# Performance work log

Hardware: AMD Instinct MI355X
Metric: run time of the kernel (lower is better)

Reference implementation:

```python
import jax, jax.numpy as jnp
import numpy as np

N_NODES = 50000
N_EDGES = 600000
D = 128
H = 256  # backbone hidden
EPS = 1e-5
NEG_SLOPE = 0.01


def setup_inputs() -> dict:
    key = jax.random.key(0)
    ks = jax.random.split(key, 16)
    s = 0.05
    inp = {
        "x": jax.random.normal(ks[0], (N_NODES, D), dtype=jnp.float32),
        "edges": jax.random.randint(ks[1], (2, N_EDGES), 0, N_NODES, dtype=jnp.int64),
        # merge layer: Linear(2D -> D), stored as (in, out)
        "merge_W": jax.random.normal(ks[2], (2 * D, D), dtype=jnp.float32) * s,
        "merge_b": jnp.zeros((D,), dtype=jnp.float32),
        # GRUCell params, torch layout: (3D, D) rows ordered [r, z, n]
        "gru_W_ih": jax.random.normal(ks[3], (3 * D, D), dtype=jnp.float32) * s,
        "gru_W_hh": jax.random.normal(ks[4], (3 * D, D), dtype=jnp.float32) * s,
        "gru_b_ih": jnp.zeros((3 * D,), dtype=jnp.float32),
        "gru_b_hh": jnp.zeros((3 * D,), dtype=jnp.float32),
        # backbone: Linear(D->256) + LeakyReLU + BN(256) + Linear(256->D) + LeakyReLU + BN(D)
        "W1": jax.random.normal(ks[5], (D, H), dtype=jnp.float32) * s,
        "b1": jnp.zeros((H,), dtype=jnp.float32),
        "gamma1": jnp.ones((H,), dtype=jnp.float32),
        "beta1": jnp.zeros((H,), dtype=jnp.float32),
        "W2": jax.random.normal(ks[6], (H, D), dtype=jnp.float32) * s,
        "b2": jnp.zeros((D,), dtype=jnp.float32),
        "gamma2": jnp.ones((D,), dtype=jnp.float32),
        "beta2": jnp.zeros((D,), dtype=jnp.float32),
    }
    return inp


def _batch_norm(y, gamma, beta):
    m = jnp.mean(y, axis=0)
    v = jnp.mean((y - m) ** 2, axis=0)  # biased var, training mode
    return gamma * (y - m) * jax.lax.rsqrt(v + EPS) + beta


def _leaky_relu(y):
    return jnp.where(y >= 0, y, NEG_SLOPE * y)


def reference(x, edges, merge_W, merge_b, gru_W_ih, gru_W_hh, gru_b_ih, gru_b_hh,
              W1, b1, gamma1, beta1, W2, b2, gamma2, beta2):
    n = x.shape[0]
    src, dst = edges[0], edges[1]
    x_neighbor = x[src]  # (E, D) gather

    # aggregation: 'sum' and 'max' scatter reductions over center nodes
    agg_sum = jax.ops.segment_sum(x_neighbor, dst, num_segments=n)
    agg_max = jax.ops.segment_max(x_neighbor, dst, num_segments=n)
    agg_max = jnp.where(jnp.isfinite(agg_max), agg_max, 0.0)  # nodes with no in-edges -> 0

    # merge multiple aggregations: cat + Linear(2D -> D)
    agg = jnp.concatenate([agg_sum, agg_max], axis=-1) @ merge_W + merge_b

    # update: GRUCell(input=agg, hidden=x)
    gi = agg @ gru_W_ih.T + gru_b_ih
    gh = x @ gru_W_hh.T + gru_b_hh
    i_r, i_z, i_n = jnp.split(gi, 3, axis=-1)
    h_r, h_z, h_n = jnp.split(gh, 3, axis=-1)
    r = jax.nn.sigmoid(i_r + h_r)
    z = jax.nn.sigmoid(i_z + h_z)
    cand = jnp.tanh(i_n + r * h_n)
    h = (1.0 - z) * cand + z * x

    # backbone MLP with training-mode BatchNorm
    y = _batch_norm(_leaky_relu(h @ W1 + b1), gamma1, beta1)
    y = _batch_norm(_leaky_relu(y @ W2 + b2), gamma2, beta2)
    return y
```

## Files before the change

### kernel.cpp

```cpp
#include <hip/hip_runtime.h>
#include <hip/hip_bf16.h>
#include <math.h>

#define NN 50000
#define NE 600000
#define DD 128
#define HH 256
#define BN_EPS 1e-5f

typedef unsigned short u16;
typedef short bf16x8 __attribute__((ext_vector_type(8)));
typedef float f32x4 __attribute__((ext_vector_type(4)));

__device__ __forceinline__ u16 f2bf(float f) {
    unsigned int u = __float_as_uint(f);
    unsigned int r = (u + 0x7fffu + ((u >> 16) & 1u)) >> 16;
    return (u16)r;
}
__device__ __forceinline__ float bf2f(u16 b) {
    return __uint_as_float(((unsigned int)b) << 16);
}
#define MFMA(a, b, c) __builtin_amdgcn_mfma_f32_16x16x32_bf16((a), (b), (c), 0, 0, 0)

__global__ __launch_bounds__(256) void k_init(int* __restrict__ deg,
                                              float* __restrict__ stats) {
    int tid = blockIdx.x * 256 + threadIdx.x;
    if (tid < NN) deg[tid] = 0;
    if (tid < 768) stats[tid] = 0.f;
}

__global__ __launch_bounds__(256) void k_count(const int* __restrict__ edges,
                                               int* __restrict__ deg) {
    int e = blockIdx.x * 256 + threadIdx.x;
    if (e >= NE) return;
    atomicAdd(&deg[edges[NE + e]], 1);
}

__global__ __launch_bounds__(256) void k_scanA(const int* __restrict__ deg,
                                               int* __restrict__ loc,
                                               int* __restrict__ bsum) {
    __shared__ int s[256];
    int b = blockIdx.x, t = threadIdx.x;
    int i0 = b * 512 + t * 2;
    int d0 = (i0 < NN) ? deg[i0] : 0;
    int d1 = (i0 + 1 < NN) ? deg[i0 + 1] : 0;
    s[t] = d0 + d1;
    __syncthreads();
    for (int off = 1; off < 256; off <<= 1) {
        int v = (t >= off) ? s[t - off] : 0;
        __syncthreads();
        s[t] += v;
        __syncthreads();
    }
    int excl = (t > 0) ? s[t - 1] : 0;
    if (i0 < NN) loc[i0] = excl;
    if (i0 + 1 < NN) loc[i0 + 1] = excl + d0;
    if (t == 255) bsum[b] = s[255];
}

__global__ __launch_bounds__(128) void k_scanB(const int* __restrict__ bsum,
                                               int* __restrict__ boff) {
    __shared__ int s[128];
    int t = threadIdx.x;
    const int NBLK = (NN + 511) / 512;
    s[t] = (t < NBLK) ? bsum[t] : 0;
    __syncthreads();
    for (int off = 1; off < 128; off <<= 1) {
        int v = (t >= off) ? s[t - off] : 0;
        __syncthreads();
        s[t] += v;
        __syncthreads();
    }
    if (t < NBLK) boff[t] = (t > 0) ? s[t - 1] : 0;
}

__global__ __launch_bounds__(256) void k_scanC(const int* __restrict__ loc,
                                               const int* __restrict__ boff,
                                               int* __restrict__ rowptr,
                                               int* __restrict__ cursor) {
    int i = blockIdx.x * 256 + threadIdx.x;
    if (i < NN) {
        int v = loc[i] + boff[i >> 9];
        rowptr[i] = v;
        cursor[i] = v;
    }
    if (i == 0) rowptr[NN] = NE;
}

__global__ __launch_bounds__(256) void k_fill(const int* __restrict__ edges,
                                              int* __restrict__ cursor,
                                              int* __restrict__ eidx) {
    int e = blockIdx.x * 256 + threadIdx.x;
    if (e >= NE) return;
    int src = edges[e];
    int dst = edges[NE + e];
    int slot = atomicAdd(&cursor[dst], 1);
    eidx[slot] = src;
}

__global__ __launch_bounds__(256) void k_xcast(const float4* __restrict__ x4,
                                               uint4* __restrict__ xb4) {
    int tid = blockIdx.x * 256 + threadIdx.x;
    if (tid >= NN * DD / 8) return;
    float4 a = x4[tid * 2];
    float4 b = x4[tid * 2 + 1];
    uint4 o;
    o.x = (unsigned)f2bf(a.x) | ((unsigned)f2bf(a.y) << 16);
    o.y = (unsigned)f2bf(a.z) | ((unsigned)f2bf(a.w) << 16);
    o.z = (unsigned)f2bf(b.x) | ((unsigned)f2bf(b.y) << 16);
    o.w = (unsigned)f2bf(b.z) | ((unsigned)f2bf(b.w) << 16);
    xb4[tid] = o;
}

__global__ __launch_bounds__(256) void k_aggregate(const unsigned* __restrict__ xb,
        const int* __restrict__ rowptr, const int* __restrict__ eidx,
        unsigned* __restrict__ asum, unsigned* __restrict__ amax) {
    int gid = blockIdx.x * 256 + threadIdx.x;
    int node = gid >> 6;
    int lane = threadIdx.x & 63;
    if (node >= NN) return;
    int beg = rowptr[node], end = rowptr[node + 1];
    float sx = 0.f, sy = 0.f;
    const float NINF = -__builtin_inff();
    float mx = NINF, my = NINF;
    int j = beg;
    for (; j + 4 <= end; j += 4) {
        int i0 = eidx[j], i1 = eidx[j + 1], i2 = eidx[j + 2], i3 = eidx[j + 3];
        unsigned v0 = xb[(size_t)i0 * 64 + lane];
        unsigned v1 = xb[(size_t)i1 * 64 + lane];
        unsigned v2 = xb[(size_t)i2 * 64 + lane];
        unsigned v3 = xb[(size_t)i3 * 64 + lane];
        float a0 = bf2f((u16)(v0 & 0xffff)), b0 = bf2f((u16)(v0 >> 16));
        float a1 = bf2f((u16)(v1 & 0xffff)), b1 = bf2f((u16)(v1 >> 16));
        float a2 = bf2f((u16)(v2 & 0xffff)), b2 = bf2f((u16)(v2 >> 16));
        float a3 = bf2f((u16)(v3 & 0xffff)), b3 = bf2f((u16)(v3 >> 16));
        sx += a0 + a1 + a2 + a3;
        sy += b0 + b1 + b2 + b3;
        mx = fmaxf(fmaxf(fmaxf(mx, a0), fmaxf(a1, a2)), a3);
        my = fmaxf(fmaxf(fmaxf(my, b0), fmaxf(b1, b2)), b3);
    }
    for (; j < end; ++j) {
        int src = eidx[j];
        unsigned v = xb[(size_t)src * 64 + lane];
        float vx = bf2f((u16)(v & 0xffff));
        float vy = bf2f((u16)(v >> 16));
        sx += vx; sy += vy;
        mx = fmaxf(mx, vx); my = fmaxf(my, vy);
    }
    if (beg == end) { mx = 0.f; my = 0.f; }
    asum[(size_t)node * 64 + lane] = (unsigned)f2bf(sx) | ((unsigned)f2bf(sy) << 16);
    amax[(size_t)node * 64 + lane] = (unsigned)f2bf(mx) | ((unsigned)f2bf(my) << 16);
}

__device__ __forceinline__ size_t packB(int k, int n, int KT) {
    int nt = n >> 4;
    int kt = k >> 5;
    int lane = (n & 15) | (((k >> 3) & 3) << 4);
    int e = k & 7;
    return ((size_t)(nt * KT + kt) * 64 + lane) * 8 + e;
}

__global__ __launch_bounds__(256) void k_prep_w(const float* __restrict__ merge_W,
        const float* __restrict__ W_ih, const float* __restrict__ W_hh,
        const float* __restrict__ merge_b,
        const float* __restrict__ b_ih, const float* __restrict__ b_hh,
        const float* __restrict__ W1,
        u16* __restrict__ Wp, float* __restrict__ bg, u16* __restrict__ W1p) {
    int bid = blockIdx.x, t = threadIdx.x;
    if (bid < 768) {
        int tid = bid * 256 + t;
        int k = tid >> 9;
        int jout = tid & 511;
        float v = 0.f;
        if (jout < 256) {
            int j = jout;
            if (k < 256) {
                float acc = 0.f;
                for (int q = 0; q < DD; ++q) acc += merge_W[k * DD + q] * W_ih[j * DD + q];
                v = acc;
            } else v = W_hh[j * DD + (k - 256)];
        } else if (jout < 384) {
            int j = jout;
            if (k < 256) {
                float acc = 0.f;
                for (int q = 0; q < DD; ++q) acc += merge_W[k * DD + q] * W_ih[j * DD + q];
                v = acc;
            }
        } else {
            int j = jout - 128;
            if (k >= 256) v = W_hh[j * DD + (k - 256)];
        }
        Wp[packB(k, jout, 12)] = f2bf(v);
    } else if (bid < 770) {
        int jout = (bid - 768) * 256 + t;
        float v;
        if (jout < 384) {
            int j = jout;
            float acc = b_ih[j];
            for (int q = 0; q < DD; ++q) acc += merge_b[q] * W_ih[j * DD + q];
            v = (jout < 256) ? acc + b_hh[j] : acc;
        } else {
            v = b_hh[jout - 128];
        }
        bg[jout] = v;
    } else {
        int tid = (bid - 770) * 256 + t;
        int k = tid >> 8;
        int j = tid & 255;
        W1p[packB(k, j, 4)] = f2bf(W1[tid]);
    }
}

__global__ __launch_bounds__(256) void k_gru_mlp1(const u16* __restrict__ asum,
        const u16* __restrict__ amax, const u16* __restrict__ xb,
        const u16* __restrict__ Wp, const float* __restrict__ bg,
        const u16* __restrict__ W1p, const float* __restrict__ b1,
        u16* __restrict__ s1, float* __restrict__ sum1, float* __restrict__ sumsq1) {
    __shared__ u16 U[32 * 392];
    __shared__ u16 HS[32 * 136];
    int t = threadIdx.x;
    int r0 = blockIdx.x * 32;
    int w = t >> 6, l = t & 63;

    #pragma unroll
    for (int src = 0; src < 3; ++src) {
        const u16* p = (src == 0) ? asum : (src == 1) ? amax : xb;
        #pragma unroll
        for (int it = 0; it < 2; ++it) {
            int i = t + it * 256;
            int row = i >> 4, c = i & 15;
            uint4 v = make_uint4(0, 0, 0, 0);
            if (r0 + row < NN) v = *(const uint4*)(p + (size_t)(r0 + row) * DD + c * 8);
            *(uint4*)(&U[row * 392 + src * DD + c * 8]) = v;
        }
    }
    __syncthreads();

    {
        f32x4 acc[2][4][2];
        #pragma unroll
        for (int mt = 0; mt < 2; ++mt)
            #pragma unroll
            for (int g = 0; g < 4; ++g)
                #pragma unroll
                for (int q = 0; q < 2; ++q) acc[mt][g][q] = (f32x4){0.f, 0.f, 0.f, 0.f};

        for (int kt = 0; kt < 12; ++kt) {
            bf16x8 a0 = *(const bf16x8*)(&U[((l & 15)) * 392 + kt * 32 + (l >> 4) * 8]);
            bf16x8 a1 = *(const bf16x8*)(&U[(16 + (l & 15)) * 392 + kt * 32 + (l >> 4) * 8]);
            #pragma unroll
            for (int g = 0; g < 4; ++g) {
                #pragma unroll
                for (int q = 0; q < 2; ++q) {
                    int nt = g * 8 + 2 * w + q;
                    bf16x8 b = *(const bf16x8*)(Wp + ((size_t)(nt * 12 + kt) * 64 + l) * 8);
                    acc[0][g][q] = MFMA(a0, b, acc[0][g][q]);
                    acc[1][g][q] = MFMA(a1, b, acc[1][g][q]);
                }
            }
        }

        #pragma unroll
        for (int mt = 0; mt < 2; ++mt) {
            #pragma unroll
            for (int q = 0; q < 2; ++q) {
                int dl = (2 * w + q) * 16 + (l & 15);
                float br = bg[dl], bz = bg[128 + dl], bi = bg[256 + dl], bh = bg[384 + dl];
                #pragma unroll
                for (int j = 0; j < 4; ++j) {
                    int row = mt * 16 + (l >> 4) * 4 + j;
                    float rp = acc[mt][0][q][j] + br;
                    float zp = acc[mt][1][q][j] + bz;
                    float ip = acc[mt][2][q][j] + bi;
                    float hp = acc[mt][3][q][j] + bh;
                    float r = 1.f / (1.f + __expf(-rp));
                    float z = 1.f / (1.f + __expf(-zp));
                    float n = tanhf(ip + r * hp);
                    float xv = bf2f(U[row * 392 + 2 * DD + dl]);
                    float h = (1.f - z) * n + z * xv;
                    HS[row * 136 + dl] = f2bf(h);
                }
            }
        }
    }
    __syncthreads();

    {
        f32x4 acc[2][4];
        #pragma unroll
        for (int mt = 0; mt < 2; ++mt)
            #pragma unroll
            for (int nl = 0; nl < 4; ++nl) acc[mt][nl] = (f32x4){0.f, 0.f, 0.f, 0.f};

        for (int kt = 0; kt < 4; ++kt) {
            bf16x8 a0 = *(const bf16x8*)(&HS[((l & 15)) * 136 + kt * 32 + (l >> 4) * 8]);
            bf16x8 a1 = *(const bf16x8*)(&HS[(16 + (l & 15)) * 136 + kt * 32 + (l >> 4) * 8]);
            #pragma unroll
            for (int nl = 0; nl < 4; ++nl) {
                int nt = w * 4 + nl;
                bf16x8 b = *(const bf16x8*)(W1p + ((size_t)(nt * 4 + kt) * 64 + l) * 8);
                acc[0][nl] = MFMA(a0, b, acc[0][nl]);
                acc[1][nl] = MFMA(a1, b, acc[1][nl]);
            }
        }

        #pragma unroll
        for (int nl = 0; nl < 4; ++nl) {
            int dcol = (w * 4 + nl) * 16 + (l & 15);
            float bj = b1[dcol];
            float cs = 0.f, cq = 0.f;
            #pragma unroll
            for (int mt = 0; mt < 2; ++mt) {
                #pragma unroll
                for (int j = 0; j < 4; ++j) {
                    int row = mt * 16 + (l >> 4) * 4 + j;
                    float v = acc[mt][nl][j] + bj;
                    v = (v >= 0.f) ? v : 0.01f * v;
                    if (r0 + row < NN) {
                        s1[(size_t)(r0 + row) * HH + dcol] = f2bf(v);
                        cs += v; cq += v * v;
                    }
                }
            }
            cs += __shfl_xor(cs, 16); cs += __shfl_xor(cs, 32);
            cq += __shfl_xor(cq, 16); cq += __shfl_xor(cq, 32);
            if (l < 16) {
                atomicAdd(&sum1[dcol], cs);
                atomicAdd(&sumsq1[dcol], cq);
            }
        }
    }
}

__global__ __launch_bounds__(256) void k_prep2(const float* __restrict__ sum1,
        const float* __restrict__ sumsq1,
        const float* __restrict__ gamma1, const float* __restrict__ beta1,
        const float* __restrict__ W2, const float* __restrict__ b2,
        u16* __restrict__ W2p, float* __restrict__ b2p) {
    __shared__ float a1s[HH], c1s[HH];
    int t = threadIdx.x;
    {
        float m = sum1[t] * (1.f / NN);
        float var = sumsq1[t] * (1.f / NN) - m * m;
        float a = gamma1[t] * rsqrtf(var + BN_EPS);
        a1s[t] = a;
        c1s[t] = beta1[t] - a * m;
    }
    __syncthreads();
    if (blockIdx.x < 128) {
        int idx = blockIdx.x * 256 + t;
        int k = idx >> 7, j = idx & 127;
        W2p[packB(k, j, 8)] = f2bf(a1s[k] * W2[k * DD + j]);
    } else if (t < DD) {
        float acc = b2[t];
        for (int k = 0; k < HH; ++k) acc = fmaf(c1s[k], W2[k * DD + t], acc);
        b2p[t] = acc;
    }
}

__global__ __launch_bounds__(256) void k_mlp2(const u16* __restrict__ s1,
        const u16* __restrict__ W2p, const float* __restrict__ b2p,
        float* __restrict__ s2, float* __restrict__ sum2, float* __restrict__ sumsq2) {
    __shared__ u16 A[32 * 264];
    int t = threadIdx.x;
    int r0 = blockIdx.x * 32;
    int w = t >> 6, l = t & 63;

    #pragma unroll
    for (int it = 0; it < 4; ++it) {
        int i = t + it * 256;
        int row = i >> 5, c = i & 31;
        uint4 v = make_uint4(0, 0, 0, 0);
        if (r0 + row < NN) v = *(const uint4*)(s1 + (size_t)(r0 + row) * HH + c * 8);
        *(uint4*)(&A[row * 264 + c * 8]) = v;
    }
    __syncthreads();

    f32x4 acc[2][2];
    #pragma unroll
    for (int mt = 0; mt < 2; ++mt)
        #pragma unroll
        for (int q = 0; q < 2; ++q) acc[mt][q] = (f32x4){0.f, 0.f, 0.f, 0.f};

    for (int kt = 0; kt < 8; ++kt) {
        bf16x8 a0 = *(const bf16x8*)(&A[((l & 15)) * 264 + kt * 32 + (l >> 4) * 8]);
        bf16x8 a1 = *(const bf16x8*)(&A[(16 + (l & 15)) * 264 + kt * 32 + (l >> 4) * 8]);
        #pragma unroll
        for (int q = 0; q < 2; ++q) {
            int nt = w * 2 + q;
            bf16x8 b = *(const bf16x8*)(W2p + ((size_t)(nt * 8 + kt) * 64 + l) * 8);
            acc[0][q] = MFMA(a0, b, acc[0][q]);
            acc[1][q] = MFMA(a1, b, acc[1][q]);
        }
    }

    #pragma unroll
    for (int q = 0; q < 2; ++q) {
        int dcol = (w * 2 + q) * 16 + (l & 15);
        float bj = b2p[dcol];
        float cs = 0.f, cq = 0.f;
        #pragma unroll
        for (int mt = 0; mt < 2; ++mt) {
            #pragma unroll
            for (int j = 0; j < 4; ++j) {
                int row = mt * 16 + (l >> 4) * 4 + j;
                float v = acc[mt][q][j] + bj;
                v = (v >= 0.f) ? v : 0.01f * v;
                if (r0 + row < NN) {
                    s2[(size_t)(r0 + row) * DD + dcol] = v;
                    cs += v; cq += v * v;
                }
            }
        }
        cs += __shfl_xor(cs, 16); cs += __shfl_xor(cs, 32);
        cq += __shfl_xor(cq, 16); cq += __shfl_xor(cq, 32);
        if (l < 16) {
            atomicAdd(&sum2[dcol], cs);
            atomicAdd(&sumsq2[dcol], cq);
        }
    }
}

__global__ __launch_bounds__(256) void k_bn_out(const float* __restrict__ s2,
        const float* __restrict__ sum2, const float* __restrict__ sumsq2,
        const float* __restrict__ gamma2, const float* __restrict__ beta2,
        float* __restrict__ out) {
    __shared__ float a2s[DD], c2s[DD];
    int t = threadIdx.x;
    if (t < DD) {
        float m = sum2[t] * (1.f / NN);
        float var = sumsq2[t] * (1.f / NN) - m * m;
        float a = gamma2[t] * rsqrtf(var + BN_EPS);
        a2s[t] = a;
        c2s[t] = beta2[t] - a * m;
    }
    __syncthreads();
    int tid = blockIdx.x * 256 + t;
    if (tid >= NN * DD / 4) return;
    int c4 = (tid & 31) * 4;
    float4 v = ((const float4*)s2)[tid];
    float4 o;
    o.x = a2s[c4 + 0] * v.x + c2s[c4 + 0];
    o.y = a2s[c4 + 1] * v.y + c2s[c4 + 1];
    o.z = a2s[c4 + 2] * v.z + c2s[c4 + 2];
    o.w = a2s[c4 + 3] * v.w + c2s[c4 + 3];
    ((float4*)out)[tid] = o;
}

extern "C" void kernel_launch(void* const* d_in, const int* in_sizes, int n_in,
                              void* d_out, int out_size, void* d_ws, size_t ws_size,
                              hipStream_t stream) {
    const float* x       = (const float*)d_in[0];
    const int*   edges   = (const int*)d_in[1];
    const float* merge_W = (const float*)d_in[2];
    const float* merge_b = (const float*)d_in[3];
    const float* W_ih    = (const float*)d_in[4];
    const float* W_hh    = (const float*)d_in[5];
    const float* b_ih    = (const float*)d_in[6];
    const float* b_hh    = (const float*)d_in[7];
    const float* W1      = (const float*)d_in[8];
    const float* b1      = (const float*)d_in[9];
    const float* gamma1  = (const float*)d_in[10];
    const float* beta1   = (const float*)d_in[11];
    const float* W2      = (const float*)d_in[12];
    const float* b2      = (const float*)d_in[13];
    const float* gamma2  = (const float*)d_in[14];
    const float* beta2   = (const float*)d_in[15];
    float* out = (float*)d_out;

    char* wsb = (char*)d_ws;
    u16*   xb     = (u16*)(wsb + 0);
    u16*   asumb  = (u16*)(wsb + 12800000);
    u16*   amaxb  = (u16*)(wsb + 25600000);
    float* s2     = (float*)(wsb + 12800000);
    u16*   s1b    = (u16*)(wsb + 38400000);
    u16*   Wpg    = (u16*)(wsb + 64000000);
    u16*   W1p    = (u16*)(wsb + 64393216);
    u16*   W2p    = (u16*)(wsb + 64458752);
    float* bg     = (float*)(wsb + 64524288);
    float* b2p    = (float*)(wsb + 64526336);
    float* stats  = (float*)(wsb + 64526848);
    float* sum1   = stats;
    float* sumsq1 = stats + 256;
    float* sum2   = stats + 512;
    float* sumsq2 = stats + 640;
    int*   deg    = (int*)(wsb + 64529920);
    int*   rowptr = (int*)(wsb + 64729920);
    int*   cursor = (int*)(wsb + 64929924);
    int*   eidx   = (int*)(wsb + 65129924);
    int*   bsum   = (int*)(wsb + 67529924);
    int*   boff   = (int*)(wsb + 67530316);

    const int NB = (NN + 31) / 32;
    const int NBLK = (NN + 511) / 512;

    k_init<<<(NN + 255) / 256, 256, 0, stream>>>(deg, stats);
    k_count<<<(NE + 255) / 256, 256, 0, stream>>>(edges, deg);
    k_scanA<<<NBLK, 256, 0, stream>>>(deg, deg, bsum);
    k_scanB<<<1, 128, 0, stream>>>(bsum, boff);
    k_scanC<<<(NN + 255) / 256, 256, 0, stream>>>(deg, boff, rowptr, cursor);
    k_fill<<<(NE + 255) / 256, 256, 0, stream>>>(edges, cursor, eidx);
    k_xcast<<<(NN * DD / 8 + 255) / 256, 256, 0, stream>>>((const float4*)x, (uint4*)xb);
    k_prep_w<<<898, 256, 0, stream>>>(merge_W, W_ih, W_hh, merge_b, b_ih, b_hh, W1,
                                      Wpg, bg, W1p);
    k_aggregate<<<(NN * 64) / 256 + 1, 256, 0, stream>>>((const unsigned*)xb, rowptr, eidx,
                                                         (unsigned*)asumb, (unsigned*)amaxb);
    k_gru_mlp1<<<NB, 256, 0, stream>>>(asumb, amaxb, xb, Wpg, bg, W1p, b1,
                                       s1b, sum1, sumsq1);
    k_prep2<<<129, 256, 0, stream>>>(sum1, sumsq1, gamma1, beta1, W2, b2, W2p, b2p);
    k_mlp2<<<NB, 256, 0, stream>>>(s1b, W2p, b2p, s2, sum2, sumsq2);
    k_bn_out<<<6250, 256, 0, stream>>>(s2, sum2, sumsq2, gamma2, beta2, out);
}
```

Before: 399.7 us.

## Widen GRU and MLP GEMM tiles to 64 rows with 8 waves per block

The GRU+MLP1 and MLP2 GEMM kernels now process 64 rows per block with 512 threads instead of 32 rows with 256. Each wave covers one 16-column slice across four row tiles, so each weight fragment loaded from global memory is reused across four MFMAs instead of two. B fragments are loaded ahead and the k-loop is unrolled by two to expose more independent loads. The cost is more LDS and more registers per block, and about half as many blocks, which may reduce occupancy and latency hiding.

```diff
diff --git a/kernel.cpp b/kernel.cpp
--- a/kernel.cpp
+++ b/kernel.cpp
@@ -211,15 +211,15 @@
     }
 }
 
-__global__ __launch_bounds__(256) void k_gru_mlp1(const u16* __restrict__ asum,
+__global__ __launch_bounds__(512, 4) void k_gru_mlp1(const u16* __restrict__ asum,
         const u16* __restrict__ amax, const u16* __restrict__ xb,
         const u16* __restrict__ Wp, const float* __restrict__ bg,
         const u16* __restrict__ W1p, const float* __restrict__ b1,
         u16* __restrict__ s1, float* __restrict__ sum1, float* __restrict__ sumsq1) {
-    __shared__ u16 U[32 * 392];
-    __shared__ u16 HS[32 * 136];
+    __shared__ u16 U[64 * 392];
+    __shared__ u16 HS[64 * 136];
     int t = threadIdx.x;
-    int r0 = blockIdx.x * 32;
+    int r0 = blockIdx.x * 64;
     int w = t >> 6, l = t & 63;
 
     #pragma unroll
@@ -227,7 +227,7 @@
         const u16* p = (src == 0) ? asum : (src == 1) ? amax : xb;
         #pragma unroll
         for (int it = 0; it < 2; ++it) {
-            int i = t + it * 256;
+            int i = t + it * 512;
             int row = i >> 4, c = i & 15;
             uint4 v = make_uint4(0, 0, 0, 0);
             if (r0 + row < NN) v = *(const uint4*)(p + (size_t)(r0 + row) * DD + c * 8);
@@ -237,80 +237,88 @@
     __syncthreads();
 
     {
-        f32x4 acc[2][4][2];
-        #pragma unroll
-        for (int mt = 0; mt < 2; ++mt)
-            #pragma unroll
-            for (int g = 0; g < 4; ++g)
+        f32x4 acc[4][4];
+        #pragma unroll
+        for (int mt = 0; mt < 4; ++mt)
+            #pragma unroll
+            for (int g = 0; g < 4; ++g) acc[mt][g] = (f32x4){0.f, 0.f, 0.f, 0.f};
+
+        #pragma unroll 2
+        for (int kt = 0; kt < 12; ++kt) {
+            bf16x8 b[4];
+            #pragma unroll
+            for (int g = 0; g < 4; ++g) {
+                int nt = g * 8 + w;
+                b[g] = *(const bf16x8*)(Wp + ((size_t)(nt * 12 + kt) * 64 + l) * 8);
+            }
+            bf16x8 a[4];
+            #pragma unroll
+            for (int mt = 0; mt < 4; ++mt)
+                a[mt] = *(const bf16x8*)(&U[(mt * 16 + (l & 15)) * 392 + kt * 32 + (l >> 4) * 8]);
+            #pragma unroll
+            for (int mt = 0; mt < 4; ++mt) {
                 #pragma unroll
-                for (int q = 0; q < 2; ++q) acc[mt][g][q] = (f32x4){0.f, 0.f, 0.f, 0.f};
-
-        for (int kt = 0; kt < 12; ++kt) {
-            bf16x8 a0 = *(const bf16x8*)(&U[((l & 15)) * 392 + kt * 32 + (l >> 4) * 8]);
-            bf16x8 a1 = *(const bf16x8*)(&U[(16 + (l & 15)) * 392 + kt * 32 + (l >> 4) * 8]);
-            #pragma unroll
-            for (int g = 0; g < 4; ++g) {
+                for (int g = 0; g < 4; ++g)
+                    acc[mt][g] = MFMA(a[mt], b[g], acc[mt][g]);
+            }
+        }
+
+        int dl = w * 16 + (l & 15);
+        float br = bg[dl], bz = bg[128 + dl], bi = bg[256 + dl], bh = bg[384 + dl];
+        #pragma unroll
+        for (int mt = 0; mt < 4; ++mt) {
+            #pragma unroll
+            for (int j = 0; j < 4; ++j) {
+                int row = mt * 16 + (l >> 4) * 4 + j;
+                float rp = acc[mt][0][j] + br;
+                float zp = acc[mt][1][j] + bz;
+                float ip = acc[mt][2][j] + bi;
+                float hp = acc[mt][3][j] + bh;
+                float r = 1.f / (1.f + __expf(-rp));
+                float z = 1.f / (1.f + __expf(-zp));
+                float n = tanhf(ip + r * hp);
+                float xv = bf2f(U[row * 392 + 2 * DD + dl]);
+                float h = (1.f - z) * n + z * xv;
+                HS[row * 136 + dl] = f2bf(h);
+            }
+        }
+    }
+    __syncthreads();
+
+    {
+        f32x4 acc[4][2];
+        #pragma unroll
+        for (int mt = 0; mt < 4; ++mt)
+            #pragma unroll
+            for (int nl = 0; nl < 2; ++nl) acc[mt][nl] = (f32x4){0.f, 0.f, 0.f, 0.f};
+
+        #pragma unroll 2
+        for (int kt = 0; kt < 4; ++kt) {
+            bf16x8 b[2];
+            #pragma unroll
+            for (int nl = 0; nl < 2; ++nl) {
+                int nt = w * 2 + nl;
+                b[nl] = *(const bf16x8*)(W1p + ((size_t)(nt * 4 + kt) * 64 + l) * 8);
+            }
+            bf16x8 a[4];
+            #pragma unroll
+            for (int mt = 0; mt < 4; ++mt)
+                a[mt] = *(const bf16x8*)(&HS[(mt * 16 + (l & 15)) * 136 + kt * 32 + (l >> 4) * 8]);
+            #pragma unroll
+            for (int mt = 0; mt < 4; ++mt) {
                 #pragma unroll
-                for (int q = 0; q < 2; ++q) {
-                    int nt = g * 8 + 2 * w + q;
-                    bf16x8 b = *(const bf16x8*)(Wp + ((size_t)(nt * 12 + kt) * 64 + l) * 8);
-                    acc[0][g][q] = MFMA(a0, b, acc[0][g][q]);
-                    acc[1][g][q] = MFMA(a1, b, acc[1][g][q]);
-                }
-            }
-        }
-
-        #pragma unroll
-        for (int mt = 0; mt < 2; ++mt) {
-            #pragma unroll
-            for (int q = 0; q < 2; ++q) {
-                int dl = (2 * w + q) * 16 + (l & 15);
-                float br = bg[dl], bz = bg[128 + dl], bi = bg[256 + dl], bh = bg[384 + dl];
-                #pragma unroll
-                for (int j = 0; j < 4; ++j) {
-                    int row = mt * 16 + (l >> 4) * 4 + j;
-                    float rp = acc[mt][0][q][j] + br;
-                    float zp = acc[mt][1][q][j] + bz;
-                    float ip = acc[mt][2][q][j] + bi;
-                    float hp = acc[mt][3][q][j] + bh;
-                    float r = 1.f / (1.f + __expf(-rp));
-                    float z = 1.f / (1.f + __expf(-zp));
-                    float n = tanhf(ip + r * hp);
-                    float xv = bf2f(U[row * 392 + 2 * DD + dl]);
-                    float h = (1.f - z) * n + z * xv;
-                    HS[row * 136 + dl] = f2bf(h);
-                }
-            }
-        }
-    }
-    __syncthreads();
-
-    {
-        f32x4 acc[2][4];
-        #pragma unroll
-        for (int mt = 0; mt < 2; ++mt)
-            #pragma unroll
-            for (int nl = 0; nl < 4; ++nl) acc[mt][nl] = (f32x4){0.f, 0.f, 0.f, 0.f};
-
-        for (int kt = 0; kt < 4; ++kt) {
-            bf16x8 a0 = *(const bf16x8*)(&HS[((l & 15)) * 136 + kt * 32 + (l >> 4) * 8]);
-            bf16x8 a1 = *(const bf16x8*)(&HS[(16 + (l & 15)) * 136 + kt * 32 + (l >> 4) * 8]);
-            #pragma unroll
-            for (int nl = 0; nl < 4; ++nl) {
-                int nt = w * 4 + nl;
-                bf16x8 b = *(const bf16x8*)(W1p + ((size_t)(nt * 4 + kt) * 64 + l) * 8);
-                acc[0][nl] = MFMA(a0, b, acc[0][nl]);
-                acc[1][nl] = MFMA(a1, b, acc[1][nl]);
-            }
-        }
-
-        #pragma unroll
-        for (int nl = 0; nl < 4; ++nl) {
-            int dcol = (w * 4 + nl) * 16 + (l & 15);
+                for (int nl = 0; nl < 2; ++nl)
+                    acc[mt][nl] = MFMA(a[mt], b[nl], acc[mt][nl]);
+            }
+        }
+
+        #pragma unroll
+        for (int nl = 0; nl < 2; ++nl) {
+            int dcol = (w * 2 + nl) * 16 + (l & 15);
             float bj = b1[dcol];
             float cs = 0.f, cq = 0.f;
             #pragma unroll
-            for (int mt = 0; mt < 2; ++mt) {
+            for (int mt = 0; mt < 4; ++mt) {
                 #pragma unroll
                 for (int j = 0; j < 4; ++j) {
                     int row = mt * 16 + (l >> 4) * 4 + j;
@@ -358,17 +366,17 @@
     }
 }
 
-__global__ __launch_bounds__(256) void k_mlp2(const u16* __restrict__ s1,
+__global__ __launch_bounds__(512, 4) void k_mlp2(const u16* __restrict__ s1,
         const u16* __restrict__ W2p, const float* __restrict__ b2p,
         float* __restrict__ s2, float* __restrict__ sum2, float* __restrict__ sumsq2) {
-    __shared__ u16 A[32 * 264];
+    __shared__ u16 A[64 * 264];
     int t = threadIdx.x;
-    int r0 = blockIdx.x * 32;
+    int r0 = blockIdx.x * 64;
     int w = t >> 6, l = t & 63;
 
     #pragma unroll
     for (int it = 0; it < 4; ++it) {
-        int i = t + it * 256;
+        int i = t + it * 512;
         int row = i >> 5, c = i & 31;
         uint4 v = make_uint4(0, 0, 0, 0);
         if (r0 + row < NN) v = *(const uint4*)(s1 + (size_t)(r0 + row) * HH + c * 8);
@@ -376,48 +384,43 @@
     }
     __syncthreads();
 
-    f32x4 acc[2][2];
+    f32x4 acc[4];
     #pragma unroll
-    for (int mt = 0; mt < 2; ++mt)
-        #pragma unroll
-        for (int q = 0; q < 2; ++q) acc[mt][q] = (f32x4){0.f, 0.f, 0.f, 0.f};
-
+    for (int mt = 0; mt < 4; ++mt) acc[mt] = (f32x4){0.f, 0.f, 0.f, 0.f};
+
+    #pragma unroll 2
     for (int kt = 0; kt < 8; ++kt) {
-        bf16x8 a0 = *(const bf16x8*)(&A[((l & 15)) * 264 + kt * 32 + (l >> 4) * 8]);
-        bf16x8 a1 = *(const bf16x8*)(&A[(16 + (l & 15)) * 264 + kt * 32 + (l >> 4) * 8]);
-        #pragma unroll
-        for (int q = 0; q < 2; ++q) {
-            int nt = w * 2 + q;
-            bf16x8 b = *(const bf16x8*)(W2p + ((size_t)(nt * 8 + kt) * 64 + l) * 8);
-            acc[0][q] = MFMA(a0, b, acc[0][q]);
-            acc[1][q] = MFMA(a1, b, acc[1][q]);
-        }
-    }
-
+        bf16x8 b = *(const bf16x8*)(W2p + ((size_t)(w * 8 + kt) * 64 + l) * 8);
+        bf16x8 a[4];
+        #pragma unroll
+        for (int mt = 0; mt < 4; ++mt)
+            a[mt] = *(const bf16x8*)(&A[(mt * 16 + (l & 15)) * 264 + kt * 32 + (l >> 4) * 8]);
+        #pragma unroll
+        for (int mt = 0; mt < 4; ++mt)
+            acc[mt] = MFMA(a[mt], b, acc[mt]);
+    }
+
+    int dcol = w * 16 + (l & 15);
+    float bj = b2p[dcol];
+    float cs = 0.f, cq = 0.f;
     #pragma unroll
-    for (int q = 0; q < 2; ++q) {
-        int dcol = (w * 2 + q) * 16 + (l & 15);
-        float bj = b2p[dcol];
-        float cs = 0.f, cq = 0.f;
-        #pragma unroll
-        for (int mt = 0; mt < 2; ++mt) {
-            #pragma unroll
-            for (int j = 0; j < 4; ++j) {
-                int row = mt * 16 + (l >> 4) * 4 + j;
-                float v = acc[mt][q][j] + bj;
-                v = (v >= 0.f) ? v : 0.01f * v;
-                if (r0 + row < NN) {
-                    s2[(size_t)(r0 + row) * DD + dcol] = v;
-                    cs += v; cq += v * v;
-                }
-            }
-        }
-        cs += __shfl_xor(cs, 16); cs += __shfl_xor(cs, 32);
-        cq += __shfl_xor(cq, 16); cq += __shfl_xor(cq, 32);
-        if (l < 16) {
-            atomicAdd(&sum2[dcol], cs);
-            atomicAdd(&sumsq2[dcol], cq);
-        }
+    for (int mt = 0; mt < 4; ++mt) {
+        #pragma unroll
+        for (int j = 0; j < 4; ++j) {
+            int row = mt * 16 + (l >> 4) * 4 + j;
+            float v = acc[mt][j] + bj;
+            v = (v >= 0.f) ? v : 0.01f * v;
+            if (r0 + row < NN) {
+                s2[(size_t)(r0 + row) * DD + dcol] = v;
+                cs += v; cq += v * v;
+            }
+        }
+    }
+    cs += __shfl_xor(cs, 16); cs += __shfl_xor(cs, 32);
+    cq += __shfl_xor(cq, 16); cq += __shfl_xor(cq, 32);
+    if (l < 16) {
+        atomicAdd(&sum2[dcol], cs);
+        atomicAdd(&sumsq2[dcol], cq);
     }
 }
 
@@ -491,7 +494,7 @@
     int*   bsum   = (int*)(wsb + 67529924);
     int*   boff   = (int*)(wsb + 67530316);
 
-    const int NB = (NN + 31) / 32;
+    const int NB64 = (NN + 63) / 64;
     const int NBLK = (NN + 511) / 512;
 
     k_init<<<(NN + 255) / 256, 256, 0, stream>>>(deg, stats);
@@ -505,9 +508,9 @@
                                       Wpg, bg, W1p);
     k_aggregate<<<(NN * 64) / 256 + 1, 256, 0, stream>>>((const unsigned*)xb, rowptr, eidx,
                                                          (unsigned*)asumb, (unsigned*)amaxb);
-    k_gru_mlp1<<<NB, 256, 0, stream>>>(asumb, amaxb, xb, Wpg, bg, W1p, b1,
-                                       s1b, sum1, sumsq1);
+    k_gru_mlp1<<<NB64, 512, 0, stream>>>(asumb, amaxb, xb, Wpg, bg, W1p, b1,
+                                         s1b, sum1, sumsq1);
     k_prep2<<<129, 256, 0, stream>>>(sum1, sumsq1, gamma1, beta1, W2, b2, W2p, b2p);
-    k_mlp2<<<NB, 256, 0, stream>>>(s1b, W2p, b2p, s2, sum2, sumsq2);
+    k_mlp2<<<NB64, 512, 0, stream>>>(s1b, W2p, b2p, s2, sum2, sumsq2);
     k_bn_out<<<6250, 256, 0, stream>>>(s2, sum2, sumsq2, gamma2, beta2, out);
 }
```

After: 323.1 us. 1.24x faster.
